# Performance work log

Measured on AMD Instinct MI355X. Metric: run time of the kernel, lower is better.

Reference implementation:

```python
import jax, jax.numpy as jnp
import numpy as np

B, T, E, H, R = 4, 256, 128, 8, 64
D = E // H


def _xavier(k, fan_in, fan_out, gain=1.0):
    a = gain * np.sqrt(6.0 / (fan_in + fan_out))
    return jax.random.uniform(k, (fan_in, fan_out), minval=-a, maxval=a, dtype=jnp.float32)


def setup_inputs() -> dict:
    key = jax.random.key(0)
    ks = jax.random.split(key, 16)
    g = 1.0 / np.sqrt(2.0)  # gain used for q/k/v when qkv_same_dim
    return {
        "query": jax.random.normal(ks[0], (B, T, E), jnp.float32),
        "velocity": jax.random.normal(ks[1], (B, T, 3, E), jnp.float32),
        "edge_feature": jax.random.normal(ks[2], (B, T, T, R), jnp.float32),
        "edge_direction": jax.random.normal(ks[3], (B, T, T, 3), jnp.float32),
        "cutoff": jax.random.uniform(ks[4], (B, T, T), jnp.float32),
        "Wq": _xavier(ks[5], E, E, g), "bq": jnp.zeros((E,), jnp.float32),
        "Wk": _xavier(ks[6], E, E, g), "bk": jnp.zeros((E,), jnp.float32),
        "Wv": _xavier(ks[7], E, 3 * E, g), "bv": jnp.zeros((3 * E,), jnp.float32),
        "Wo": _xavier(ks[8], E, 3 * E), "bo": jnp.zeros((3 * E,), jnp.float32),
        "Wvel": _xavier(ks[9], E, 3 * E), "bvel": jnp.zeros((3 * E,), jnp.float32),
        "Wdk": _xavier(ks[10], R, E), "bdk": jnp.zeros((E,), jnp.float32),
        "Wdv": _xavier(ks[11], R, 3 * E), "bdv": jnp.zeros((3 * E,), jnp.float32),
    }


def reference(query, velocity, edge_feature, edge_direction, cutoff,
              Wq, bq, Wk, bk, Wv, bv, Wo, bo, Wvel, bvel, Wdk, bdk, Wdv, bdv):
    b, t, e = query.shape
    h = H
    d = e // h
    scaling = d ** -0.5
    # projections
    q = ((query @ Wq + bq) * scaling).reshape(b, t, 1, h, d)   # [b,t,1,h,d]
    k = (query @ Wk + bk).reshape(b, 1, t, h, d)                # [b,1,t,h,d]
    v = (query @ Wv + bv).reshape(b, 1, t, h, 3 * d)            # [b,1,t,h,3d]
    # RBF distance gates (dense pairwise)
    dk = jax.nn.silu(edge_feature @ Wdk + bdk).reshape(b, t, t, h, d)
    dv = jax.nn.silu(edge_feature @ Wdv + bdv).reshape(b, t, t, h, 3 * d)
    v = v * dv                                                  # [b,t,t,h,3d]
    v, vp1, vp2 = jnp.split(v, 3, axis=-1)                      # each [b,t,t,h,d]
    # velocity channel
    velp = velocity @ Wvel + bvel                               # [b,t,3,3e]
    w1, w2, w3 = jnp.split(velp, 3, axis=-1)                    # each [b,t,3,e]
    velocity_dot = (w1 * w2).sum(axis=2)                        # [b,t,e]
    vel_r = velocity.reshape(b, t, 3, h, d)
    # elementwise (non-dot-product) attention weights
    aw = q * k * dk / np.float32(np.sqrt(d))                    # [b,t,t,h,d]
    awf = jnp.nan_to_num(jax.nn.softmax(aw, axis=2))
    c = cutoff[..., None, None]                                 # [b,t,t,1,1]
    attn = (awf * c * v * (c != 0)).sum(axis=2).reshape(b, t, e)
    o1, o2, o3 = jnp.split(attn @ Wo + bo, 3, axis=-1)          # each [b,t,e]
    # equivariant vector path
    vec1 = vel_r[:, None] * vp1[:, :, :, None]                  # [b,t,t,3,h,d]
    vec2 = vp2[:, :, :, None] * edge_direction[..., None, None]
    vec = ((vec1 + vec2).reshape(b, t, t, 3, e) * (c != 0)).sum(axis=2)  # [b,t,3,e]
    dx = velocity_dot * o2 + o3                                 # [b,t,e]
    dvec = w3 * o1[:, :, None, :] + vec                         # [b,t,3,e]
    return dx, dvec
```

## Files before the change

kernel.cpp:

```cpp
#include <hip/hip_runtime.h>
#include <hip/hip_bf16.h>
#include <math.h>

#define TT 256
#define EE 128
#define TJ 16
#define SRCW 896
#define SRCB 28672

typedef __attribute__((ext_vector_type(8))) short short8v;
typedef __attribute__((ext_vector_type(4))) float f32x4;

__device__ __forceinline__ float silu_f(float x) {
    return x * __builtin_amdgcn_rcpf(1.0f + __expf(-x));
}

__device__ __forceinline__ unsigned short f2bf(float f) {
    union { float f; unsigned u; } x; x.f = f;
    unsigned r = (x.u + 0x7FFFu + ((x.u >> 16) & 1u)) >> 16;
    return (unsigned short)r;
}

__device__ __forceinline__ unsigned cvt_pk_bf16(float lo, float hi) {
    unsigned r;
    asm("v_cvt_pk_bf16_f32 %0, %1, %2" : "=v"(r) : "v"(lo), "v"(hi));
    return r;
}

__device__ __forceinline__ float bflo(unsigned u) { return __uint_as_float(u << 16); }
__device__ __forceinline__ float bfhi(unsigned u) { return __uint_as_float(u & 0xffff0000u); }
__device__ __forceinline__ float bfu(unsigned short u) { return __uint_as_float(((unsigned)u) << 16); }

__global__ __launch_bounds__(256) void packW_kernel(
    const float* __restrict__ Wdk, const float* __restrict__ Wdv,
    unsigned short* __restrict__ wfrag) {
    const int idx = blockIdx.x * 256 + threadIdx.x;
    const int lane = idx & 63;
    const int kh = (idx >> 6) & 1;
    const int nn = (idx >> 7) & 7;
    const int w = idx >> 10;
    const float* Wsel; int wstride, colbase;
    if (w == 0) { Wsel = Wdk; wstride = 128; colbase = 0; }
    else { Wsel = Wdv; wstride = 384; colbase = (w - 1) * 128; }
    const int lrow = lane >> 4;
    const int lcol = lane & 15;
    const int col = colbase + nn * 16 + lcol;
    unsigned short* dst = wfrag + (size_t)idx * 8;
#pragma unroll
    for (int e = 0; e < 8; ++e) {
        const int k = kh * 32 + lrow * 8 + e;
        dst[e] = f2bf(Wsel[k * wstride + col]);
    }
}

__global__ __launch_bounds__(256) void phaseA_kernel(
    const float* __restrict__ query, const float* __restrict__ velocity,
    const float* __restrict__ Wq, const float* __restrict__ bq,
    const float* __restrict__ Wk, const float* __restrict__ bk,
    const float* __restrict__ Wv, const float* __restrict__ bv,
    const float* __restrict__ Wvel, const float* __restrict__ bvel,
    float* __restrict__ qs_ws, unsigned short* __restrict__ kkvv,
    float* __restrict__ veldot_ws, float* __restrict__ w3_ws) {
    const int row = blockIdx.x;
    const int t = threadIdx.x;
    __shared__ float sIn[EE];
    __shared__ float sVel[3 * EE];
    __shared__ float sVelp[3 * 384];
    if (t < EE) sIn[t] = query[(size_t)row * EE + t];
    for (int idx = t; idx < 3 * EE; idx += 256)
        sVel[idx] = velocity[(size_t)row * 3 * EE + idx];
    __syncthreads();

    unsigned short* krow = kkvv + (size_t)row * SRCW;
    for (int o = t; o < 640; o += 256) {
        if (o < 128) {
            int c = o;
            float acc = bq[c];
#pragma unroll 8
            for (int r = 0; r < 128; ++r) acc = fmaf(sIn[r], Wq[r * 128 + c], acc);
            qs_ws[(size_t)row * 128 + c] = acc * 0.25f;
        } else if (o < 256) {
            int c = o - 128;
            float acc = bk[c];
#pragma unroll 8
            for (int r = 0; r < 128; ++r) acc = fmaf(sIn[r], Wk[r * 128 + c], acc);
            krow[c] = f2bf(acc);
        } else {
            int c = o - 256;
            float acc = bv[c];
#pragma unroll 8
            for (int r = 0; r < 128; ++r) acc = fmaf(sIn[r], Wv[r * 384 + c], acc);
            krow[128 + c] = f2bf(acc);
        }
    }
    for (int idx = t; idx < 384; idx += 256)
        krow[512 + idx] = f2bf(sVel[idx]);

    for (int c = t; c < 384; c += 256) {
        float a0 = bvel[c], a1 = a0, a2 = a0;
#pragma unroll 8
        for (int r = 0; r < 128; ++r) {
            float w = Wvel[r * 384 + c];
            a0 = fmaf(sVel[r], w, a0);
            a1 = fmaf(sVel[128 + r], w, a1);
            a2 = fmaf(sVel[256 + r], w, a2);
        }
        sVelp[0 * 384 + c] = a0;
        sVelp[1 * 384 + c] = a1;
        sVelp[2 * 384 + c] = a2;
    }
    __syncthreads();
    if (t < 128) {
        int c = t;
        float vd = 0.f;
#pragma unroll
        for (int s = 0; s < 3; ++s)
            vd += sVelp[s * 384 + c] * sVelp[s * 384 + 128 + c];
        veldot_ws[(size_t)row * 128 + c] = vd;
#pragma unroll
        for (int s = 0; s < 3; ++s)
            w3_ws[((size_t)row * 3 + s) * 128 + c] = sVelp[s * 384 + 256 + c];
    }
}

__global__ __launch_bounds__(256, 2) void phaseB_kernel(
    const float* __restrict__ edge_feature, const float* __restrict__ edge_direction,
    const float* __restrict__ cutoff,
    const unsigned short* __restrict__ wfrag, const unsigned short* __restrict__ kkvv,
    const float* __restrict__ bdk, const float* __restrict__ bdv,
    const float* __restrict__ qs_ws,
    float* __restrict__ attn_ws, float* __restrict__ vec_ws) {
    const int blk = blockIdx.x;
    const int x = blk & 7;
    const int slot = blk >> 3;
    const int b = x >> 1;
    const int i = ((x & 1) << 7) + slot;
    const int row = b * TT + i;

    const int t = threadIdx.x;
    const int wave = t >> 6;
    const int lane = t & 63;
    const int lrow = lane >> 4;
    const int lcol = lane & 15;

    __shared__ __align__(16) unsigned char sSrc[2 * SRCB];
    __shared__ __align__(16) unsigned char sEFb[16 * 128];
    __shared__ unsigned short sKD[128 * 18];
    __shared__ unsigned short sGV[3 * 128 * 18];
    __shared__ float sCut[TJ];
    __shared__ float sDirS[TJ * 3];
    __shared__ float sMrg[128][5];

    const float* Bsel;
    int colbase;
    if (wave == 0) { Bsel = bdk; colbase = 0; }
    else { Bsel = bdv; colbase = (wave - 1) * 128; }

    float biasv[8];
#pragma unroll
    for (int n = 0; n < 8; ++n)
        biasv[n] = Bsel[colbase + n * 16 + lcol];

    const unsigned short* wfbase = wfrag + ((size_t)wave * 1024 + lane) * 8;
    const int gobase = (wave == 0) ? 0 : 128;

    const int grp = t >> 7;
    const int c = t & 127;
    const float qsc = qs_ws[(size_t)row * 128 + c] * 0.25f;

    float l = 0.f, A = 0.f;
    float v0 = 0.f, v1 = 0.f, v2 = 0.f;

    const size_t ef_base = (size_t)row * TT * 64;
    const size_t cut_base = (size_t)row * TT;
    const size_t dir_base = (size_t)row * TT * 3;
    const unsigned char* kvbase = (const unsigned char*)kkvv + (size_t)(b * TT) * 1792;

    const int ldsoff = (t & 192) * 16;

#pragma unroll
    for (int r = 0; r < 7; ++r)
        __builtin_amdgcn_global_load_lds(
            (const void*)(kvbase + (size_t)r * 4096 + (size_t)t * 16),
            (void*)(sSrc + r * 4096 + ldsoff), 16, 0, 0);

    f32x4 pEf = ((const f32x4*)(edge_feature + ef_base))[t];
    float pCut = (t < TJ) ? cutoff[cut_base + t] : 0.f;
    float pDir = (t < TJ * 3) ? edge_direction[dir_base + t] : 0.f;

    int p = 0;
    for (int j0 = 0; j0 < TT; j0 += TJ) {
        {
            const int erow = t >> 4;
            const int kq = t & 15;
            unsigned plo = cvt_pk_bf16(pEf[0], pEf[1]);
            unsigned phi = cvt_pk_bf16(pEf[2], pEf[3]);
            const int byteoff = (kq * 8) ^ ((erow & 7) << 4);
            *(int2*)(sEFb + erow * 128 + byteoff) = make_int2((int)plo, (int)phi);
            if (t < TJ) sCut[t] = pCut;
            if (t < TJ * 3) sDirS[t] = pDir;
        }
        __syncthreads();

        if (j0 + TJ < TT) {
            const unsigned char* src = kvbase + (size_t)(j0 + TJ) * 1792;
            unsigned char* dst = sSrc + (p ^ 1) * SRCB;
#pragma unroll
            for (int r = 0; r < 7; ++r)
                __builtin_amdgcn_global_load_lds(
                    (const void*)(src + (size_t)r * 4096 + (size_t)t * 16),
                    (void*)(dst + r * 4096 + ldsoff), 16, 0, 0);
        }
        {
            const int jn = (j0 + TJ) & 255;
            pEf = ((const f32x4*)(edge_feature + ef_base + (size_t)jn * 64))[t];
            pCut = (t < TJ) ? cutoff[cut_base + jn + t] : 0.f;
            pDir = (t < TJ * 3) ? edge_direction[dir_base + (size_t)jn * 3 + t] : 0.f;
        }

        {
            const unsigned short* srow = (const unsigned short*)(sSrc + p * SRCB);
            const int arow = lcol;
            const int swzb = (arow & 7) << 4;
            const short8v a0 = *(const short8v*)(sEFb + arow * 128 + ((lrow * 16) ^ swzb));
            const short8v a1 = *(const short8v*)(sEFb + arow * 128 + ((64 + lrow * 16) ^ swzb));
            const int ljb = lrow * 4;
#pragma unroll
            for (int n = 0; n < 8; ++n) {
                const int col = colbase + n * 16 + lcol;
                const unsigned short* gp = srow + (size_t)ljb * SRCW + gobase + col;
                const float g0 = bfu(gp[0]);
                const float g1 = bfu(gp[SRCW]);
                const float g2 = bfu(gp[2 * SRCW]);
                const float g3 = bfu(gp[3 * SRCW]);
                const short8v b0 = *(const short8v*)(wfbase + (size_t)n * 1024);
                const short8v b1 = *(const short8v*)(wfbase + (size_t)n * 1024 + 512);
                f32x4 acc = {biasv[n], biasv[n], biasv[n], biasv[n]};
                acc = __builtin_amdgcn_mfma_f32_16x16x32_bf16(a0, b0, acc, 0, 0, 0);
                acc = __builtin_amdgcn_mfma_f32_16x16x32_bf16(a1, b1, acc, 0, 0, 0);
                const float r0 = g0 * silu_f(acc[0]);
                const float r1 = g1 * silu_f(acc[1]);
                const float r2 = g2 * silu_f(acc[2]);
                const float r3 = g3 * silu_f(acc[3]);
                const unsigned w01 = cvt_pk_bf16(r0, r1);
                const unsigned w23 = cvt_pk_bf16(r2, r3);
                unsigned short* dst;
                if (wave == 0) {
                    dst = &sKD[col * 18 + lrow * 4];
                } else {
                    const int plane = (col >> 4) % 3;
                    const int cch = (col / 48) * 16 + lcol;
                    dst = &sGV[plane * 2304 + cch * 18 + lrow * 4];
                }
                *(unsigned*)(dst) = w01;
                *(unsigned*)(dst + 2) = w23;
            }
        }
        __syncthreads();

        {
            const unsigned short* srow = (const unsigned short*)(sSrc + p * SRCB);
            const int jlo = grp * (TJ / 2);
#pragma unroll
            for (int q = 0; q < 4; ++q) {
                const int jj = jlo + 2 * q;
                const unsigned kd2 = *(const unsigned*)(&sKD[c * 18 + jj]);
                const unsigned vg2 = *(const unsigned*)(&sGV[0 * 2304 + c * 18 + jj]);
                const unsigned p12 = *(const unsigned*)(&sGV[1 * 2304 + c * 18 + jj]);
                const unsigned p22 = *(const unsigned*)(&sGV[2 * 2304 + c * 18 + jj]);
                const float cut0 = sCut[jj];
                const float cut1 = sCut[jj + 1];
                const float p0 = __expf(qsc * bflo(kd2));
                const float p1 = __expf(qsc * bfhi(kd2));
                l += p0 + p1;
                A = fmaf(p0 * cut0, bflo(vg2), A);
                A = fmaf(p1 * cut1, bfhi(vg2), A);
                if (cut0 != 0.0f) {
                    const unsigned short* vp = srow + (size_t)jj * SRCW + 512 + c;
                    const float w1 = bflo(p12), w2 = bflo(p22);
                    v0 = fmaf(bfu(vp[0]),   w1, fmaf(w2, sDirS[jj * 3 + 0], v0));
                    v1 = fmaf(bfu(vp[128]), w1, fmaf(w2, sDirS[jj * 3 + 1], v1));
                    v2 = fmaf(bfu(vp[256]), w1, fmaf(w2, sDirS[jj * 3 + 2], v2));
                }
                if (cut1 != 0.0f) {
                    const unsigned short* vp = srow + (size_t)(jj + 1) * SRCW + 512 + c;
                    const float w1 = bfhi(p12), w2 = bfhi(p22);
                    v0 = fmaf(bfu(vp[0]),   w1, fmaf(w2, sDirS[jj * 3 + 3], v0));
                    v1 = fmaf(bfu(vp[128]), w1, fmaf(w2, sDirS[jj * 3 + 4], v1));
                    v2 = fmaf(bfu(vp[256]), w1, fmaf(w2, sDirS[jj * 3 + 5], v2));
                }
            }
        }
        __syncthreads();
        p ^= 1;
    }

    if (grp == 1) {
        sMrg[c][0] = l;  sMrg[c][1] = A;
        sMrg[c][2] = v0; sMrg[c][3] = v1; sMrg[c][4] = v2;
    }
    __syncthreads();
    if (grp == 0) {
        const float L = l + sMrg[c][0];
        const float Aa = A + sMrg[c][1];
        const float attn = (L > 0.f) ? (Aa * __builtin_amdgcn_rcpf(L)) : 0.f;
        attn_ws[(size_t)row * 128 + c] = attn;
        vec_ws[((size_t)row * 3 + 0) * 128 + c] = v0 + sMrg[c][2];
        vec_ws[((size_t)row * 3 + 1) * 128 + c] = v1 + sMrg[c][3];
        vec_ws[((size_t)row * 3 + 2) * 128 + c] = v2 + sMrg[c][4];
    }
}

__global__ __launch_bounds__(256) void phaseC_kernel(
    const float* __restrict__ Wo, const float* __restrict__ bo,
    const float* __restrict__ attn_ws, const float* __restrict__ veldot_ws,
    const float* __restrict__ w3_ws, const float* __restrict__ vec_ws,
    float* __restrict__ out) {
    const int row = blockIdx.x;
    const int t = threadIdx.x;
    __shared__ float sAttn[128];
    __shared__ float sO[384];
    if (t < 128) sAttn[t] = attn_ws[(size_t)row * 128 + t];
    __syncthreads();
    for (int o = t; o < 384; o += 256) {
        float acc = bo[o];
#pragma unroll 8
        for (int r = 0; r < 128; ++r) acc = fmaf(sAttn[r], Wo[r * 384 + o], acc);
        sO[o] = acc;
    }
    __syncthreads();
    if (t < 128) {
        int c = t;
        float o1 = sO[c], o2 = sO[128 + c], o3 = sO[256 + c];
        float dx = fmaf(veldot_ws[(size_t)row * 128 + c], o2, o3);
        out[(size_t)row * 128 + c] = dx;
#pragma unroll
        for (int s = 0; s < 3; ++s) {
            size_t idx = ((size_t)row * 3 + s) * 128 + c;
            out[131072 + idx] = fmaf(w3_ws[idx], o1, vec_ws[idx]);
        }
    }
}

extern "C" void kernel_launch(void* const* d_in, const int* in_sizes, int n_in,
                              void* d_out, int out_size, void* d_ws, size_t ws_size,
                              hipStream_t stream) {
    (void)in_sizes; (void)n_in; (void)out_size; (void)ws_size;
    const float* query          = (const float*)d_in[0];
    const float* velocity       = (const float*)d_in[1];
    const float* edge_feature   = (const float*)d_in[2];
    const float* edge_direction = (const float*)d_in[3];
    const float* cutoff         = (const float*)d_in[4];
    const float* Wq   = (const float*)d_in[5];  const float* bq   = (const float*)d_in[6];
    const float* Wk   = (const float*)d_in[7];  const float* bk   = (const float*)d_in[8];
    const float* Wv   = (const float*)d_in[9];  const float* bv   = (const float*)d_in[10];
    const float* Wo   = (const float*)d_in[11]; const float* bo   = (const float*)d_in[12];
    const float* Wvel = (const float*)d_in[13]; const float* bvel = (const float*)d_in[14];
    const float* Wdk  = (const float*)d_in[15]; const float* bdk  = (const float*)d_in[16];
    const float* Wdv  = (const float*)d_in[17]; const float* bdv  = (const float*)d_in[18];

    float* ws        = (float*)d_ws;
    float* qs_ws     = ws;
    float* veldot_ws = ws + 131072;
    float* w3_ws     = ws + 262144;
    float* attn_ws   = ws + 655360;
    float* vec_ws    = ws + 786432;
    unsigned short* wfrag = (unsigned short*)(ws + 1179648);
    unsigned short* kkvv  = (unsigned short*)(ws + 1196032);

    float* out = (float*)d_out;

    hipLaunchKernelGGL(packW_kernel, dim3(16), dim3(256), 0, stream,
        Wdk, Wdv, wfrag);
    hipLaunchKernelGGL(phaseA_kernel, dim3(1024), dim3(256), 0, stream,
        query, velocity, Wq, bq, Wk, bk, Wv, bv, Wvel, bvel,
        qs_ws, kkvv, veldot_ws, w3_ws);
    hipLaunchKernelGGL(phaseB_kernel, dim3(1024), dim3(256), 0, stream,
        edge_feature, edge_direction, cutoff,
        wfrag, kkvv, bdk, bdv, qs_ws, attn_ws, vec_ws);
    hipLaunchKernelGGL(phaseC_kernel, dim3(1024), dim3(256), 0, stream,
        Wo, bo, attn_ws, veldot_ws, w3_ws, vec_ws, out);
}
```

Before: 164.0 us.

## Transpose k/v staging layout per 16-row tile and keep MFMA weights in registers

Phase A now writes the bf16 k/v projections in a per-16-row tiled transposed layout, with the velocity block stored after them. Phase B can then read the four j-values per column as one 8-byte LDS load instead of four strided scalar loads. The B-matrix weight fragments for the MFMA are also loaded once into registers before the loop instead of from global memory every tile. This raises register pressure (16 short8 vectors) under a launch bound of 2 blocks and changes the LDS access pattern, which may add bank conflicts.

```diff
diff --git a/kernel.cpp b/kernel.cpp
--- a/kernel.cpp
+++ b/kernel.cpp
@@ -5,10 +5,11 @@
 #define TT 256
 #define EE 128
 #define TJ 16
-#define SRCW 896
 #define SRCB 28672
+#define TSH 14336
 
 typedef __attribute__((ext_vector_type(8))) short short8v;
+typedef __attribute__((ext_vector_type(4))) short short4v;
 typedef __attribute__((ext_vector_type(4))) float f32x4;
 
 __device__ __forceinline__ float silu_f(float x) {
@@ -59,7 +60,7 @@
     const float* __restrict__ Wk, const float* __restrict__ bk,
     const float* __restrict__ Wv, const float* __restrict__ bv,
     const float* __restrict__ Wvel, const float* __restrict__ bvel,
-    float* __restrict__ qs_ws, unsigned short* __restrict__ kkvv,
+    float* __restrict__ qs_ws, unsigned short* __restrict__ kkvvT,
     float* __restrict__ veldot_ws, float* __restrict__ w3_ws) {
     const int row = blockIdx.x;
     const int t = threadIdx.x;
@@ -71,7 +72,8 @@
         sVel[idx] = velocity[(size_t)row * 3 * EE + idx];
     __syncthreads();
 
-    unsigned short* krow = kkvv + (size_t)row * SRCW;
+    unsigned short* tb = kkvvT + (size_t)(row >> 4) * TSH;
+    const int r16 = row & 15;
     for (int o = t; o < 640; o += 256) {
         if (o < 128) {
             int c = o;
@@ -84,17 +86,17 @@
             float acc = bk[c];
 #pragma unroll 8
             for (int r = 0; r < 128; ++r) acc = fmaf(sIn[r], Wk[r * 128 + c], acc);
-            krow[c] = f2bf(acc);
+            tb[c * 16 + r16] = f2bf(acc);
         } else {
             int c = o - 256;
             float acc = bv[c];
 #pragma unroll 8
             for (int r = 0; r < 128; ++r) acc = fmaf(sIn[r], Wv[r * 384 + c], acc);
-            krow[128 + c] = f2bf(acc);
+            tb[(128 + c) * 16 + r16] = f2bf(acc);
         }
     }
     for (int idx = t; idx < 384; idx += 256)
-        krow[512 + idx] = f2bf(sVel[idx]);
+        tb[8192 + r16 * 384 + idx] = f2bf(sVel[idx]);
 
     for (int c = t; c < 384; c += 256) {
         float a0 = bvel[c], a1 = a0, a2 = a0;
@@ -126,7 +128,7 @@
 __global__ __launch_bounds__(256, 2) void phaseB_kernel(
     const float* __restrict__ edge_feature, const float* __restrict__ edge_direction,
     const float* __restrict__ cutoff,
-    const unsigned short* __restrict__ wfrag, const unsigned short* __restrict__ kkvv,
+    const unsigned short* __restrict__ wfrag, const unsigned short* __restrict__ kkvvT,
     const float* __restrict__ bdk, const float* __restrict__ bdv,
     const float* __restrict__ qs_ws,
     float* __restrict__ attn_ws, float* __restrict__ vec_ws) {
@@ -162,7 +164,12 @@
         biasv[n] = Bsel[colbase + n * 16 + lcol];
 
     const unsigned short* wfbase = wfrag + ((size_t)wave * 1024 + lane) * 8;
-    const int gobase = (wave == 0) ? 0 : 128;
+    short8v bwr[16];
+#pragma unroll
+    for (int n = 0; n < 8; ++n) {
+        bwr[2 * n]     = *(const short8v*)(wfbase + (size_t)n * 1024);
+        bwr[2 * n + 1] = *(const short8v*)(wfbase + (size_t)n * 1024 + 512);
+    }
 
     const int grp = t >> 7;
     const int c = t & 127;
@@ -174,14 +181,14 @@
     const size_t ef_base = (size_t)row * TT * 64;
     const size_t cut_base = (size_t)row * TT;
     const size_t dir_base = (size_t)row * TT * 3;
-    const unsigned char* kvbase = (const unsigned char*)kkvv + (size_t)(b * TT) * 1792;
+    const unsigned char* kvT = (const unsigned char*)kkvvT + (size_t)(b * 16) * SRCB;
 
     const int ldsoff = (t & 192) * 16;
 
 #pragma unroll
     for (int r = 0; r < 7; ++r)
         __builtin_amdgcn_global_load_lds(
-            (const void*)(kvbase + (size_t)r * 4096 + (size_t)t * 16),
+            (const void*)(kvT + (size_t)r * 4096 + (size_t)t * 16),
             (void*)(sSrc + r * 4096 + ldsoff), 16, 0, 0);
 
     f32x4 pEf = ((const f32x4*)(edge_feature + ef_base))[t];
@@ -203,7 +210,7 @@
         __syncthreads();
 
         if (j0 + TJ < TT) {
-            const unsigned char* src = kvbase + (size_t)(j0 + TJ) * 1792;
+            const unsigned char* src = kvT + (size_t)((j0 >> 4) + 1) * SRCB;
             unsigned char* dst = sSrc + (p ^ 1) * SRCB;
 #pragma unroll
             for (int r = 0; r < 7; ++r)
@@ -219,29 +226,26 @@
         }
 
         {
-            const unsigned short* srow = (const unsigned short*)(sSrc + p * SRCB);
+            const unsigned short* gT = (const unsigned short*)(sSrc + p * SRCB);
             const int arow = lcol;
             const int swzb = (arow & 7) << 4;
             const short8v a0 = *(const short8v*)(sEFb + arow * 128 + ((lrow * 16) ^ swzb));
             const short8v a1 = *(const short8v*)(sEFb + arow * 128 + ((64 + lrow * 16) ^ swzb));
-            const int ljb = lrow * 4;
+
+            short4v g4[8];
+#pragma unroll
+            for (int n = 0; n < 8; ++n)
+                g4[n] = *(const short4v*)(gT + ((wave * 128 + n * 16 + lcol) * 16 + lrow * 4));
 #pragma unroll
             for (int n = 0; n < 8; ++n) {
                 const int col = colbase + n * 16 + lcol;
-                const unsigned short* gp = srow + (size_t)ljb * SRCW + gobase + col;
-                const float g0 = bfu(gp[0]);
-                const float g1 = bfu(gp[SRCW]);
-                const float g2 = bfu(gp[2 * SRCW]);
-                const float g3 = bfu(gp[3 * SRCW]);
-                const short8v b0 = *(const short8v*)(wfbase + (size_t)n * 1024);
-                const short8v b1 = *(const short8v*)(wfbase + (size_t)n * 1024 + 512);
                 f32x4 acc = {biasv[n], biasv[n], biasv[n], biasv[n]};
-                acc = __builtin_amdgcn_mfma_f32_16x16x32_bf16(a0, b0, acc, 0, 0, 0);
-                acc = __builtin_amdgcn_mfma_f32_16x16x32_bf16(a1, b1, acc, 0, 0, 0);
-                const float r0 = g0 * silu_f(acc[0]);
-                const float r1 = g1 * silu_f(acc[1]);
-                const float r2 = g2 * silu_f(acc[2]);
-                const float r3 = g3 * silu_f(acc[3]);
+                acc = __builtin_amdgcn_mfma_f32_16x16x32_bf16(a0, bwr[2 * n],     acc, 0, 0, 0);
+                acc = __builtin_amdgcn_mfma_f32_16x16x32_bf16(a1, bwr[2 * n + 1], acc, 0, 0, 0);
+                const float r0 = bfu((unsigned short)g4[n][0]) * silu_f(acc[0]);
+                const float r1 = bfu((unsigned short)g4[n][1]) * silu_f(acc[1]);
+                const float r2 = bfu((unsigned short)g4[n][2]) * silu_f(acc[2]);
+                const float r3 = bfu((unsigned short)g4[n][3]) * silu_f(acc[3]);
                 const unsigned w01 = cvt_pk_bf16(r0, r1);
                 const unsigned w23 = cvt_pk_bf16(r2, r3);
                 unsigned short* dst;
@@ -259,7 +263,7 @@
         __syncthreads();
 
         {
-            const unsigned short* srow = (const unsigned short*)(sSrc + p * SRCB);
+            const unsigned short* svel = (const unsigned short*)(sSrc + p * SRCB + 16384);
             const int jlo = grp * (TJ / 2);
 #pragma unroll
             for (int q = 0; q < 4; ++q) {
@@ -276,14 +280,14 @@
                 A = fmaf(p0 * cut0, bflo(vg2), A);
                 A = fmaf(p1 * cut1, bfhi(vg2), A);
                 if (cut0 != 0.0f) {
-                    const unsigned short* vp = srow + (size_t)jj * SRCW + 512 + c;
+                    const unsigned short* vp = svel + (size_t)jj * 384 + c;
                     const float w1 = bflo(p12), w2 = bflo(p22);
                     v0 = fmaf(bfu(vp[0]),   w1, fmaf(w2, sDirS[jj * 3 + 0], v0));
                     v1 = fmaf(bfu(vp[128]), w1, fmaf(w2, sDirS[jj * 3 + 1], v1));
                     v2 = fmaf(bfu(vp[256]), w1, fmaf(w2, sDirS[jj * 3 + 2], v2));
                 }
                 if (cut1 != 0.0f) {
-                    const unsigned short* vp = srow + (size_t)(jj + 1) * SRCW + 512 + c;
+                    const unsigned short* vp = svel + (size_t)(jj + 1) * 384 + c;
                     const float w1 = bfhi(p12), w2 = bfhi(p22);
                     v0 = fmaf(bfu(vp[0]),   w1, fmaf(w2, sDirS[jj * 3 + 3], v0));
                     v1 = fmaf(bfu(vp[128]), w1, fmaf(w2, sDirS[jj * 3 + 4], v1));
@@ -366,7 +370,7 @@
     float* attn_ws   = ws + 655360;
     float* vec_ws    = ws + 786432;
     unsigned short* wfrag = (unsigned short*)(ws + 1179648);
-    unsigned short* kkvv  = (unsigned short*)(ws + 1196032);
+    unsigned short* kkvvT = (unsigned short*)(ws + 1196032);
 
     float* out = (float*)d_out;
 
@@ -374,10 +378,10 @@
         Wdk, Wdv, wfrag);
     hipLaunchKernelGGL(phaseA_kernel, dim3(1024), dim3(256), 0, stream,
         query, velocity, Wq, bq, Wk, bk, Wv, bv, Wvel, bvel,
-        qs_ws, kkvv, veldot_ws, w3_ws);
+        qs_ws, kkvvT, veldot_ws, w3_ws);
     hipLaunchKernelGGL(phaseB_kernel, dim3(1024), dim3(256), 0, stream,
         edge_feature, edge_direction, cutoff,
-        wfrag, kkvv, bdk, bdv, qs_ws, attn_ws, vec_ws);
+        wfrag, kkvvT, bdk, bdv, qs_ws, attn_ws, vec_ws);
     hipLaunchKernelGGL(phaseC_kernel, dim3(1024), dim3(256), 0, stream,
         Wo, bo, attn_ws, veldot_ws, w3_ws, vec_ws, out);
 }
```

New measurement: 156.9 us. -4.3%, faster.
